# Kernel optimization log

Measured on AMD Instinct MI355X. Metric: run time of the kernel, lower is better.

Reference implementation:

```python
import jax, jax.numpy as jnp
import numpy as np

FEATS = [(100, 100), (50, 50), (25, 25), (13, 13)]  # (W, H) per level
BS, NQ, D = 2, 10000, 256
NH, NL, NP, G = 8, 4, 4, 8
HD = D // NH


def grid_sample_bilinear(im, grid):
    """torch.nn.functional.grid_sample(mode='bilinear', padding_mode='zeros', align_corners=False).
    im: [N, C, H, W]; grid: [N, Hg, Wg, 2] in [-1, 1] (x, y). Returns [N, C, Hg, Wg]."""
    N, C, H, W = im.shape
    Hg, Wg = grid.shape[1], grid.shape[2]
    x = (grid[..., 0] + 1.0) * (W * 0.5) - 0.5
    y = (grid[..., 1] + 1.0) * (H * 0.5) - 0.5
    x0 = jnp.floor(x); y0 = jnp.floor(y)
    wx1 = x - x0; wx0 = 1.0 - wx1
    wy1 = y - y0; wy0 = 1.0 - wy1
    imf = im.reshape(N, C, H * W)

    def corner(xi, yi, w):
        inb = (xi >= 0) & (xi < W) & (yi >= 0) & (yi < H)
        xi_c = jnp.clip(xi, 0, W - 1).astype(jnp.int32)
        yi_c = jnp.clip(yi, 0, H - 1).astype(jnp.int32)
        idx = (yi_c * W + xi_c).reshape(N, 1, Hg * Wg)
        vals = jnp.take_along_axis(imf, idx, axis=2).reshape(N, C, Hg, Wg)
        return vals * (w * inb.astype(im.dtype))[:, None]

    out = (corner(x0, y0, wx0 * wy0) + corner(x0 + 1, y0, wx1 * wy0)
           + corner(x0, y0 + 1, wx0 * wy1) + corner(x0 + 1, y0 + 1, wx1 * wy1))
    return out


def setup_inputs() -> dict:
    key = jax.random.key(0)
    ks = jax.random.split(key, 7)
    nv = sum(w * h for (w, h) in FEATS)
    return {
        "query": jax.random.normal(ks[0], (BS, NQ, D), jnp.float32),
        "value": jax.random.normal(ks[1], (BS, nv, NH, HD), jnp.float32),
        "reference_points": jax.random.uniform(ks[2], (BS, NQ, NL, 2), jnp.float32),
        "spatial_shapes": jnp.array(FEATS, jnp.float32),  # rows are (W, H)
        "W_off": jax.random.normal(ks[3], (NH * NL * NP * 2, D), jnp.float32) * 0.02,
        "b_off": jax.random.normal(ks[4], (NH * NL * NP * 2,), jnp.float32) * 0.5,
        "W_attn": jax.random.normal(ks[5], (NH * NL * NP, D), jnp.float32) * 0.02,
        "b_attn": jax.random.normal(ks[6], (NH * NL * NP,), jnp.float32) * 0.02,
    }


def reference(query, value, reference_points, spatial_shapes, W_off, b_off, W_attn, b_attn):
    bs, nq, _ = query.shape
    # sampling offsets: [bs, nq, NH, NL*NP*2] with (level, point, xy) layout
    off = (jnp.einsum('bqd,od->bqo', query, W_off) + b_off).reshape(bs, nq, NH, NL * NP * 2)
    # reference points tiled to the same (level, point, xy) layout
    ref = jnp.broadcast_to(reference_points[:, :, None, :, None, :],
                           (bs, nq, NH, NL, NP, 2)).reshape(bs, nq, NH, NL * NP * 2)
    # offset normalizer: (1/W, 1/H) per level, tiled over points
    inv = 1.0 / spatial_shapes  # [NL, 2]
    norm = jnp.broadcast_to(inv[:, None, :], (NL, NP, 2)).reshape(-1)
    loc = (ref + off * norm) * 2.0 - 1.0  # [bs, nq, NH, NL*NP*2]
    loc = loc.reshape(bs, nq, NH, NL, NP, 2)

    # attention weights: softmax over (NL*NP), then rearranged to [bs*NH, 1, nq/G, NL*G*NP]
    aw = jax.nn.softmax((jnp.einsum('bqd,od->bqo', query, W_attn) + b_attn)
                        .reshape(bs, nq, NH, NL * NP), axis=-1)
    aw = aw.reshape(bs, nq // G, G, NH, NL, NP).transpose(0, 3, 1, 4, 2, 5)
    aw = aw.reshape(bs * NH, 1, nq // G, NL * G * NP)

    # per-level grid_sample
    sizes = [w * h for (w, h) in FEATS]
    starts = np.concatenate([[0], np.cumsum(sizes)]).tolist()
    sampled = []
    for lvl, (Wl, Hl) in enumerate(FEATS):
        val_l = value[:, starts[lvl]:starts[lvl + 1]]  # [bs, Hl*Wl, NH, HD]
        val_l = val_l.transpose(0, 2, 3, 1).reshape(bs * NH, HD, Hl, Wl)
        grid_l = loc[:, :, :, lvl].transpose(0, 2, 1, 3, 4)  # [bs, NH, nq, NP, 2]
        grid_l = grid_l.reshape(bs * NH, nq // G, G * NP, 2)
        sampled.append(grid_sample_bilinear(val_l, grid_l))  # [bs*NH, HD, nq/G, G*NP]
    sv = jnp.concatenate(sampled, axis=-1)  # [bs*NH, HD, nq/G, NL*G*NP]

    out = sv * aw
    # reduce_sum linear (fixed 0/1 weight from init_weights) == sum over levels and points per group slot
    out = out.reshape(bs * NH, HD, nq // G, NL, G, NP).sum(axis=(3, 5))  # [bs*NH, HD, nq/G, G]
    return out.reshape(bs, NH * HD, nq)
```

## Files before the change

### kernel.cpp

```cpp
#include <hip/hip_runtime.h>

#define NQ   10000
#define BSZ  2
#define DIM  256
#define NH   8
#define HD   32
#define NLV  4
#define NPT  4
#define NV   13294
#define MT   (BSZ*NQ)
#define NOUT 384
#define NVAL (BSZ*NV*NH*HD)
#define GEMM_BLOCKS 939
#define PREP_BLOCKS 6647

typedef float    floatx4 __attribute__((ext_vector_type(4)));
typedef int      intx4   __attribute__((ext_vector_type(4)));
typedef __bf16   bf16x8  __attribute__((ext_vector_type(8)));
typedef _Float16 halfx8  __attribute__((ext_vector_type(8)));
typedef _Float16 halfx4  __attribute__((ext_vector_type(4)));
typedef _Float16 halfx2  __attribute__((ext_vector_type(2)));

__device__ __forceinline__ unsigned pk_bf16(float lo, float hi) {
  return __builtin_amdgcn_perm(__float_as_uint(hi) + 0x8000u,
                               __float_as_uint(lo) + 0x8000u, 0x07060302);
}

__device__ __forceinline__ unsigned short f32_to_f16_bits(float f) {
  _Float16 h = (_Float16)f;
  return __builtin_bit_cast(unsigned short, h);
}

__global__ __launch_bounds__(256) void gp_kernel(
    const float* __restrict__ query, const float* __restrict__ W_off,
    const float* __restrict__ W_attn,
    const float* __restrict__ b_off, const float* __restrict__ b_attn,
    const float* __restrict__ value,
    _Float16* __restrict__ rawh, _Float16* __restrict__ vf16) {
  const int bid = blockIdx.x;
  const int tid = threadIdx.x;
  if (bid >= GEMM_BLOCKS) {
    int i = (bid - GEMM_BLOCKS) * 256 + tid;
    if (i * 4 < NVAL) {
      floatx4 v = *(const floatx4*)&value[i * 4];
      halfx4 t = { (_Float16)v.x, (_Float16)v.y, (_Float16)v.z, (_Float16)v.w };
      *(uint2*)&vf16[i * 4] = *(const uint2*)&t;
    }
    return;
  }
  __shared__ unsigned short As[64][40];
  __shared__ unsigned short Bs[128][40];
  const int n0 = (bid % 3) * 128;
  const int m0 = (bid / 3) * 64;
  const int wave = tid >> 6;
  const int lane = tid & 63;
  const int quad = lane >> 4;
  const int l16  = lane & 15;
  floatx4 acc[8] = {};
  const int ar = tid >> 2;
  const int ac = (tid & 3) * 8;
  const int br = tid >> 1;
  const int bc = (tid & 1) * 16;
  const float* __restrict__ Wsrc =
      (n0 < 256) ? (W_off + (size_t)n0 * DIM) : (W_attn + (size_t)(n0 - 256) * DIM);

  for (int k0 = 0; k0 < DIM; k0 += 32) {
    {
      int gm = m0 + ar;
      floatx4 a0 = {}, a1 = {};
      if (gm < MT) {
        const float* src = query + (size_t)gm * DIM + k0 + ac;
        a0 = *(const floatx4*)src;
        a1 = *(const floatx4*)(src + 4);
      }
      uint4 ua = { pk_bf16(a0.x, a0.y), pk_bf16(a0.z, a0.w),
                   pk_bf16(a1.x, a1.y), pk_bf16(a1.z, a1.w) };
      *(uint4*)&As[ar][ac] = ua;
    }
    {
      const float* src = Wsrc + (size_t)br * DIM + k0 + bc;
      floatx4 b0 = *(const floatx4*)src;
      floatx4 b1 = *(const floatx4*)(src + 4);
      floatx4 b2 = *(const floatx4*)(src + 8);
      floatx4 b3 = *(const floatx4*)(src + 12);
      uint4 u0 = { pk_bf16(b0.x, b0.y), pk_bf16(b0.z, b0.w),
                   pk_bf16(b1.x, b1.y), pk_bf16(b1.z, b1.w) };
      uint4 u1 = { pk_bf16(b2.x, b2.y), pk_bf16(b2.z, b2.w),
                   pk_bf16(b3.x, b3.y), pk_bf16(b3.z, b3.w) };
      *(uint4*)&Bs[br][bc]     = u0;
      *(uint4*)&Bs[br][bc + 8] = u1;
    }
    __syncthreads();
    bf16x8 a = *(const bf16x8*)&As[wave*16 + l16][quad*8];
    #pragma unroll
    for (int nt = 0; nt < 8; nt++) {
      bf16x8 b = *(const bf16x8*)&Bs[nt*16 + l16][quad*8];
      acc[nt] = __builtin_amdgcn_mfma_f32_16x16x32_bf16(a, b, acc[nt], 0, 0, 0);
    }
    __syncthreads();
  }
  #pragma unroll
  for (int nt = 0; nt < 8; nt++) {
    int gn = n0 + nt*16 + l16;
    float bias = (gn < 256) ? b_off[gn] : b_attn[gn - 256];
    #pragma unroll
    for (int r = 0; r < 4; r++) {
      int gm = m0 + wave*16 + quad*4 + r;
      if (gm < MT) rawh[(size_t)gm*NOUT + gn] = (_Float16)(acc[nt][r] + bias);
    }
  }
}

__global__ __launch_bounds__(256) void sample_kernel(
    const _Float16* __restrict__ rawh, const _Float16* __restrict__ vf16,
    const float* __restrict__ refp, _Float16* __restrict__ tmph) {
  const int b  = blockIdx.y;
  const int q0 = blockIdx.x * 8;
  const int mbase = b * NQ + q0;
  const int tid = threadIdx.x;

  __shared__ unsigned int s_idx[64 * 34];
  __shared__ unsigned int s_w  [64 * 34];

  constexpr int WLI[4] = {100, 50, 25, 13};
  constexpr int STI[4] = {0, 10000, 12500, 13125};

  const int p   = tid & 3;
  const int r   = tid >> 2;
  const int hh  = r & 7;
  const int ql0 = r >> 3;
  const int m   = mbase + ql0;
  const _Float16* rp = rawh + (size_t)m * NOUT;

  float lg[4], rpx[4], rpy[4];
  #pragma unroll
  for (int it = 0; it < 4; ++it) {
    unsigned oxy = *(const unsigned*)(rp + hh*32 + it*8 + p*2);
    halfx2 o2 = __builtin_bit_cast(halfx2, oxy);
    lg[it] = (float)rp[256 + hh*16 + it*4 + p];
    float Wl = (float)WLI[it];
    float rx = refp[((size_t)m*NLV + it)*2 + 0];
    float ry = refp[((size_t)m*NLV + it)*2 + 1];
    rpx[it] = rx * Wl + (float)o2.x - 0.5f;
    rpy[it] = ry * Wl + (float)o2.y - 0.5f;
  }

  float mx = fmaxf(fmaxf(lg[0], lg[1]), fmaxf(lg[2], lg[3]));
  mx = fmaxf(mx, __shfl_xor(mx, 1));
  mx = fmaxf(mx, __shfl_xor(mx, 2));
  float e[4], sden = 0.f;
  #pragma unroll
  for (int it = 0; it < 4; ++it) { e[it] = __expf(lg[it] - mx); sden += e[it]; }
  sden += __shfl_xor(sden, 1);
  sden += __shfl_xor(sden, 2);
  float inv = 1.f / sden;

  #pragma unroll
  for (int it = 0; it < 4; ++it) {
    float aw = e[it] * inv;
    float px = rpx[it], py = rpy[it];
    float x0f = floorf(px), y0f = floorf(py);
    int x0 = (int)x0f, y0 = (int)y0f;
    float wx1 = px - x0f, wx0 = 1.f - wx1;
    float wy1 = py - y0f, wy0 = 1.f - wy1;
    const int Wl = WLI[it], STl = STI[it];
    unsigned short ib[4], wb[4];
    #pragma unroll
    for (int t = 0; t < 4; ++t) {
      int xi = x0 + (t & 1), yi = y0 + (t >> 1);
      bool inb = (xi >= 0) & (xi < Wl) & (yi >= 0) & (yi < Wl);
      ib[t] = inb ? (unsigned short)(STl + yi*Wl + xi) : (unsigned short)0;
      float w = inb ? (aw * ((t & 1) ? wx1 : wx0) * ((t >> 1) ? wy1 : wy0)) : 0.f;
      wb[t] = f32_to_f16_bits(w);
    }
    const int lp2 = (it*4 + p) * 2;
    uint2 ip = { (unsigned)ib[0] | ((unsigned)ib[1] << 16),
                 (unsigned)ib[2] | ((unsigned)ib[3] << 16) };
    uint2 wp = { (unsigned)wb[0] | ((unsigned)wb[1] << 16),
                 (unsigned)wb[2] | ((unsigned)wb[3] << 16) };
    *(uint2*)&s_idx[r*34 + lp2] = ip;
    *(uint2*)&s_w  [r*34 + lp2] = wp;
  }
  __syncthreads();

  const int wv = tid >> 6, lane = tid & 63;
  const int qh = lane >> 5, ql = wv*2 + qh;
  const int h = (lane >> 2) & 7, cq = lane & 3;
  const char* vbh = (const char*)vf16 + (size_t)b * (NV*NH*HD*2) + h*64 + cq*16;
  floatx4 acc0 = {0.f,0.f,0.f,0.f}, acc1 = {0.f,0.f,0.f,0.f};
  const int row = (ql*8 + h) * 34;
  #pragma unroll 4
  for (int pt = 0; pt < 16; ++pt) {
    uint2 ui = *(const uint2*)&s_idx[row + pt*2];
    uint2 wp = *(const uint2*)&s_w  [row + pt*2];
    halfx4 hw = __builtin_bit_cast(halfx4, wp);
    int o0 = (int)(ui.x & 0xffffu) << 9;
    int o1 = (int)(ui.x >> 16)     << 9;
    int o2 = (int)(ui.y & 0xffffu) << 9;
    int o3 = (int)(ui.y >> 16)     << 9;
    halfx8 v0 = *(const halfx8*)(vbh + o0);
    halfx8 v1 = *(const halfx8*)(vbh + o1);
    halfx8 v2 = *(const halfx8*)(vbh + o2);
    halfx8 v3 = *(const halfx8*)(vbh + o3);
    #pragma unroll
    for (int t = 0; t < 4; ++t) {
      halfx8 v = (t==0) ? v0 : (t==1) ? v1 : (t==2) ? v2 : v3;
      float w = (float)hw[t];
      acc0.x += w * (float)v[0];
      acc0.y += w * (float)v[1];
      acc0.z += w * (float)v[2];
      acc0.w += w * (float)v[3];
      acc1.x += w * (float)v[4];
      acc1.y += w * (float)v[5];
      acc1.z += w * (float)v[6];
      acc1.w += w * (float)v[7];
    }
  }
  int mo = mbase + ql;
  uint4 st = { __builtin_bit_cast(unsigned, __builtin_amdgcn_cvt_pkrtz(acc0.x, acc0.y)),
               __builtin_bit_cast(unsigned, __builtin_amdgcn_cvt_pkrtz(acc0.z, acc0.w)),
               __builtin_bit_cast(unsigned, __builtin_amdgcn_cvt_pkrtz(acc1.x, acc1.y)),
               __builtin_bit_cast(unsigned, __builtin_amdgcn_cvt_pkrtz(acc1.z, acc1.w)) };
  *(uint4*)&tmph[(size_t)mo * DIM + h*HD + cq*8] = st;
}

__global__ __launch_bounds__(256) void transpose_kernel(
    const _Float16* __restrict__ tmph, float* __restrict__ out) {
  __shared__ float tile[32][33];
  const int b  = blockIdx.z;
  const int q0 = blockIdx.x * 32;
  const int c0 = blockIdx.y * 32;
  const int tx = threadIdx.x & 31;
  const int ty = threadIdx.x >> 5;
  #pragma unroll
  for (int i = 0; i < 4; i++) {
    int qq = q0 + ty + i*8;
    tile[ty + i*8][tx] = (qq < NQ) ? (float)tmph[((size_t)b*NQ + qq)*DIM + c0 + tx] : 0.f;
  }
  __syncthreads();
  if (q0 + tx < NQ) {
    #pragma unroll
    for (int i = 0; i < 4; i++) {
      out[((size_t)b*DIM + c0 + ty + i*8)*NQ + q0 + tx] = tile[tx][ty + i*8];
    }
  }
}

extern "C" void kernel_launch(void* const* d_in, const int* in_sizes, int n_in,
                              void* d_out, int out_size, void* d_ws, size_t ws_size,
                              hipStream_t stream) {
  const float* query  = (const float*)d_in[0];
  const float* value  = (const float*)d_in[1];
  const float* refp   = (const float*)d_in[2];
  const float* W_off  = (const float*)d_in[4];
  const float* b_off  = (const float*)d_in[5];
  const float* W_attn = (const float*)d_in[6];
  const float* b_attn = (const float*)d_in[7];
  float* out = (float*)d_out;

  char* ws = (char*)d_ws;
  _Float16* rawh = (_Float16*)ws;
  _Float16* tmph = (_Float16*)(ws + 15360000);
  _Float16* vf16 = (_Float16*)(ws + 25600000);

  hipLaunchKernelGGL(gp_kernel, dim3(GEMM_BLOCKS + PREP_BLOCKS), dim3(256), 0, stream,
                     query, W_off, W_attn, b_off, b_attn, value, rawh, vf16);
  hipLaunchKernelGGL(sample_kernel, dim3(NQ / 8, BSZ), dim3(256), 0, stream,
                     rawh, vf16, refp, tmph);
  hipLaunchKernelGGL(transpose_kernel, dim3(313, 8, 2), dim3(256), 0, stream,
                     tmph, out);
}
```

Before: 169.3 us.

## Shrink sample kernel to single-wave blocks with packed index/weight LDS entries

The sampling kernel now runs one 64-thread wave per block over 2 queries instead of 256 threads over 8 queries, with launch bounds (64,8). The separate index and weight LDS arrays are merged into a single uint4 per point, read with one 128-bit LDS load. Smaller blocks mean the __syncthreads covers only one wave and more independent blocks can be resident to hide gather latency. The cost is four times as many blocks and extra per-block launch overhead.

```diff
diff --git a/kernel.cpp b/kernel.cpp
--- a/kernel.cpp
+++ b/kernel.cpp
@@ -111,16 +111,15 @@
   }
 }
 
-__global__ __launch_bounds__(256) void sample_kernel(
+__global__ __launch_bounds__(64, 8) void sample_kernel(
     const _Float16* __restrict__ rawh, const _Float16* __restrict__ vf16,
     const float* __restrict__ refp, _Float16* __restrict__ tmph) {
   const int b  = blockIdx.y;
-  const int q0 = blockIdx.x * 8;
+  const int q0 = blockIdx.x * 2;
   const int mbase = b * NQ + q0;
   const int tid = threadIdx.x;
 
-  __shared__ unsigned int s_idx[64 * 34];
-  __shared__ unsigned int s_w  [64 * 34];
+  __shared__ uint4 s_pk[16 * 17];
 
   constexpr int WLI[4] = {100, 50, 25, 13};
   constexpr int STI[4] = {0, 10000, 12500, 13125};
@@ -173,31 +172,29 @@
       float w = inb ? (aw * ((t & 1) ? wx1 : wx0) * ((t >> 1) ? wy1 : wy0)) : 0.f;
       wb[t] = f32_to_f16_bits(w);
     }
-    const int lp2 = (it*4 + p) * 2;
-    uint2 ip = { (unsigned)ib[0] | ((unsigned)ib[1] << 16),
-                 (unsigned)ib[2] | ((unsigned)ib[3] << 16) };
-    uint2 wp = { (unsigned)wb[0] | ((unsigned)wb[1] << 16),
+    uint4 pk = { (unsigned)ib[0] | ((unsigned)ib[1] << 16),
+                 (unsigned)ib[2] | ((unsigned)ib[3] << 16),
+                 (unsigned)wb[0] | ((unsigned)wb[1] << 16),
                  (unsigned)wb[2] | ((unsigned)wb[3] << 16) };
-    *(uint2*)&s_idx[r*34 + lp2] = ip;
-    *(uint2*)&s_w  [r*34 + lp2] = wp;
+    s_pk[r*17 + it*4 + p] = pk;
   }
   __syncthreads();
 
-  const int wv = tid >> 6, lane = tid & 63;
-  const int qh = lane >> 5, ql = wv*2 + qh;
+  const int lane = tid;
+  const int ql = lane >> 5;
   const int h = (lane >> 2) & 7, cq = lane & 3;
   const char* vbh = (const char*)vf16 + (size_t)b * (NV*NH*HD*2) + h*64 + cq*16;
   floatx4 acc0 = {0.f,0.f,0.f,0.f}, acc1 = {0.f,0.f,0.f,0.f};
-  const int row = (ql*8 + h) * 34;
+  const int rowbase = (ql*8 + h) * 17;
   #pragma unroll 4
   for (int pt = 0; pt < 16; ++pt) {
-    uint2 ui = *(const uint2*)&s_idx[row + pt*2];
-    uint2 wp = *(const uint2*)&s_w  [row + pt*2];
-    halfx4 hw = __builtin_bit_cast(halfx4, wp);
-    int o0 = (int)(ui.x & 0xffffu) << 9;
-    int o1 = (int)(ui.x >> 16)     << 9;
-    int o2 = (int)(ui.y & 0xffffu) << 9;
-    int o3 = (int)(ui.y >> 16)     << 9;
+    uint4 pk = s_pk[rowbase + pt];
+    uint2 wpair = { pk.z, pk.w };
+    halfx4 hw = __builtin_bit_cast(halfx4, wpair);
+    int o0 = (int)(pk.x & 0xffffu) << 9;
+    int o1 = (int)(pk.x >> 16)     << 9;
+    int o2 = (int)(pk.y & 0xffffu) << 9;
+    int o3 = (int)(pk.y >> 16)     << 9;
     halfx8 v0 = *(const halfx8*)(vbh + o0);
     halfx8 v1 = *(const halfx8*)(vbh + o1);
     halfx8 v2 = *(const halfx8*)(vbh + o2);
@@ -205,15 +202,15 @@
     #pragma unroll
     for (int t = 0; t < 4; ++t) {
       halfx8 v = (t==0) ? v0 : (t==1) ? v1 : (t==2) ? v2 : v3;
-      float w = (float)hw[t];
-      acc0.x += w * (float)v[0];
-      acc0.y += w * (float)v[1];
-      acc0.z += w * (float)v[2];
-      acc0.w += w * (float)v[3];
-      acc1.x += w * (float)v[4];
-      acc1.y += w * (float)v[5];
-      acc1.z += w * (float)v[6];
-      acc1.w += w * (float)v[7];
+      _Float16 wt = hw[t];
+      acc0.x += (float)wt * (float)v[0];
+      acc0.y += (float)wt * (float)v[1];
+      acc0.z += (float)wt * (float)v[2];
+      acc0.w += (float)wt * (float)v[3];
+      acc1.x += (float)wt * (float)v[4];
+      acc1.y += (float)wt * (float)v[5];
+      acc1.z += (float)wt * (float)v[6];
+      acc1.w += (float)wt * (float)v[7];
     }
   }
   int mo = mbase + ql;
@@ -265,7 +262,7 @@
 
   hipLaunchKernelGGL(gp_kernel, dim3(GEMM_BLOCKS + PREP_BLOCKS), dim3(256), 0, stream,
                      query, W_off, W_attn, b_off, b_attn, value, rawh, vf16);
-  hipLaunchKernelGGL(sample_kernel, dim3(NQ / 8, BSZ), dim3(256), 0, stream,
+  hipLaunchKernelGGL(sample_kernel, dim3(NQ / 2, BSZ), dim3(64), 0, stream,
                      rawh, vf16, refp, tmph);
   hipLaunchKernelGGL(transpose_kernel, dim3(313, 8, 2), dim3(256), 0, stream,
                      tmph, out);
```

Result: slower. 176.7 us (+4.4%).
